# Kernel tuning notes

Hardware: AMD Instinct MI355X
Metric: run time of the kernel (lower is better)

Reference implementation:

```python
import jax, jax.numpy as jnp
import numpy as np

N, M, D = 65536, 1024, 2


def setup_inputs() -> dict:
    key = jax.random.key(0)
    k1, k2, k3 = jax.random.split(key, 3)
    sample = jax.random.uniform(k1, (N, D), dtype=jnp.float32)
    mu = jax.random.uniform(k2, (M, D), dtype=jnp.float32)
    # original init: A = 10 * I; add small noise so covariances are anisotropic
    A = 10.0 * jnp.broadcast_to(jnp.eye(D, dtype=jnp.float32), (M, D, D)) \
        + 0.1 * jax.random.normal(k3, (M, D, D), dtype=jnp.float32)
    w = jnp.ones((M, 1), dtype=jnp.float32)
    return {"sample": sample, "mu": mu, "A": A, "w": w}


def reference(sample, mu, A, w):
    # gamma_j = A_j @ A_j^T  -> precision matrices, (M, D, D)
    gamma = jnp.einsum('mde,mfe->mdf', A, A)
    # 2x2 determinant (only case implemented in the original module)
    det = gamma[:, 0, 0] * gamma[:, 1, 1] - gamma[:, 0, 1] * gamma[:, 1, 0]
    # log weights: log_softmax(w) + 0.5 * log det(gamma)
    log_w = jax.nn.log_softmax(w[:, 0], axis=0) + 0.5 * jnp.log(det)  # (M,)
    # Mahalanobis quadratic form q_ij = (x_i - mu_j)^T gamma_j (x_i - mu_j),
    # expanded to avoid materializing an (N, M, D) difference tensor.
    xGx = jnp.einsum('nd,mde,ne->nm', sample, gamma, sample)          # (N, M)
    gm = jnp.einsum('mde,me->md', gamma, mu)                          # (M, D)
    cross = sample @ gm.T                                             # (N, M)
    mGm = jnp.einsum('md,md->m', gm, mu)                              # (M,)
    q = xGx - 2.0 * cross + mGm[None, :]
    # log-likelihood per sample: logsumexp_j (log_w_j - q_ij)
    return jax.nn.logsumexp(log_w[None, :] - q, axis=1)               # (N,)
```

## Files before the change

### kernel.cpp

```cpp
#include <hip/hip_runtime.h>
#include <math.h>

#define LOG2E 1.4426950408889634f
#define LN2   0.6931471805599453f

static constexpr int M = 1024;
static constexpr int N = 65536;

typedef float v2f __attribute__((ext_vector_type(2)));

__device__ inline v2f pkfma(v2f a, v2f b, v2f c) {
    v2f d;
    asm("v_pk_fma_f32 %0, %1, %2, %3" : "=v"(d) : "v"(a), "v"(b), "v"(c));
    return d;
}

__device__ inline float wave_max64(float v) {
    #pragma unroll
    for (int o = 32; o > 0; o >>= 1) v = fmaxf(v, __shfl_xor(v, o));
    return v;
}
__device__ inline float wave_sum64(float v) {
    #pragma unroll
    for (int o = 32; o > 0; o >>= 1) v += __shfl_xor(v, o);
    return v;
}

__global__ __launch_bounds__(1024)
void gm_all(const float* __restrict__ sample,
            const float* __restrict__ mu,
            const float* __restrict__ A,
            const float* __restrict__ w,
            float* __restrict__ out) {
    __shared__ __align__(16) float coef[M*6];
    __shared__ float partial[16*256];

    const int t    = threadIdx.x;
    const int lane = t & 63;
    const int wv   = t >> 6;
    const int base = blockIdx.x * 256;

    float2 s[4];
    #pragma unroll
    for (int k = 0; k < 4; ++k)
        s[k] = ((const float2*)sample)[base + 64*k + lane];

    const float4 a4  = ((const float4*)A)[t];
    const float2 mu2 = ((const float2*)mu)[t];
    const float  wt  = w[t];

    const float g00 = a4.x*a4.x + a4.y*a4.y;
    const float g01 = a4.x*a4.z + a4.y*a4.w;
    const float g11 = a4.z*a4.z + a4.w*a4.w;
    const float gm0 = g00*mu2.x + g01*mu2.y;
    const float gm1 = g01*mu2.x + g11*mu2.y;
    const float mGm = gm0*mu2.x + gm1*mu2.y;
    const float det = g00*g11 - g01*g01;
    const float t2  = wt*LOG2E + 0.5f*__builtin_amdgcn_logf(det);

    {
        float* c = coef + (t >> 1)*12 + (t & 1);
        c[0]  = t2 - LOG2E * mGm;
        c[2]  = LOG2E * 2.0f * gm0;
        c[4]  = LOG2E * 2.0f * gm1;
        c[6]  = -LOG2E * g00;
        c[8]  = -LOG2E * 2.0f * g01;
        c[10] = -LOG2E * g11;
    }

    float nlse = 0.0f;
    if (wv < 4) {
        float4 wq[4];
        #pragma unroll
        for (int i = 0; i < 4; ++i)
            wq[i] = ((const float4*)w)[lane + 64*i];
        float wmax = wq[0].x;
        #pragma unroll
        for (int i = 0; i < 4; ++i) {
            wmax = fmaxf(wmax, wq[i].x); wmax = fmaxf(wmax, wq[i].y);
            wmax = fmaxf(wmax, wq[i].z); wmax = fmaxf(wmax, wq[i].w);
        }
        wmax = wave_max64(wmax);
        float sw = 0.0f;
        #pragma unroll
        for (int i = 0; i < 4; ++i) {
            sw += __builtin_amdgcn_exp2f((wq[i].x - wmax)*LOG2E);
            sw += __builtin_amdgcn_exp2f((wq[i].y - wmax)*LOG2E);
            sw += __builtin_amdgcn_exp2f((wq[i].z - wmax)*LOG2E);
            sw += __builtin_amdgcn_exp2f((wq[i].w - wmax)*LOG2E);
        }
        sw = wave_sum64(sw);
        nlse = -(wmax*LOG2E + __builtin_amdgcn_logf(sw));
    }

    asm volatile("s_waitcnt lgkmcnt(0)" ::: "memory");
    __builtin_amdgcn_sched_barrier(0);

    v2f X[4], Y[4];
    #pragma unroll
    for (int k = 0; k < 4; ++k) {
        X[k] = (v2f){s[k].x, s[k].x};
        Y[k] = (v2f){s[k].y, s[k].y};
    }
    v2f acc[4] = {(v2f){0,0},(v2f){0,0},(v2f){0,0},(v2f){0,0}};

    const float4* cw = (const float4*)(coef + wv*64*6);
    #pragma unroll 4
    for (int p = 0; p < 32; ++p) {
        const float4 q0 = cw[p*3 + 0];
        const float4 q1 = cw[p*3 + 1];
        const float4 q2 = cw[p*3 + 2];
        const v2f c0 = {q0.x, q0.y}, c1 = {q0.z, q0.w};
        const v2f c2 = {q1.x, q1.y}, c3 = {q1.z, q1.w};
        const v2f c4 = {q2.x, q2.y}, c5 = {q2.z, q2.w};
        #pragma unroll
        for (int k = 0; k < 4; ++k) {
            v2f u  = pkfma(c3, X[k], c1);
            u      = pkfma(c4, Y[k], u);
            v2f t3 = pkfma(c5, Y[k], c2);
            v2f v  = pkfma(u,  X[k], c0);
            v      = pkfma(t3, Y[k], v);
            const float ea = __builtin_amdgcn_exp2f(v.x);
            const float eb = __builtin_amdgcn_exp2f(v.y);
            acc[k] += (v2f){ea, eb};
        }
    }

    #pragma unroll
    for (int k = 0; k < 4; ++k)
        partial[wv*256 + 64*k + lane] = acc[k].x + acc[k].y;
    __syncthreads();

    if (t < 256) {
        float ssum = partial[t];
        #pragma unroll
        for (int i = 1; i < 16; ++i) ssum += partial[i*256 + t];
        out[base + t] = LN2 * (nlse + __builtin_amdgcn_logf(ssum));
    }
}

extern "C" void kernel_launch(void* const* d_in, const int* in_sizes, int n_in,
                              void* d_out, int out_size, void* d_ws, size_t ws_size,
                              hipStream_t stream) {
    const float* sample = (const float*)d_in[0];
    const float* mu     = (const float*)d_in[1];
    const float* A      = (const float*)d_in[2];
    const float* w      = (const float*)d_in[3];
    float* out = (float*)d_out;
    (void)in_sizes; (void)n_in; (void)out_size; (void)d_ws; (void)ws_size;

    gm_all<<<256, 1024, 0, stream>>>(sample, mu, A, w, out);
}
```

Baseline: 70.22 us.

## Compute quadratic forms with bf16 MFMA using hi/lo split features

The per-pair quadratic form is rewritten as a dot product between six polynomial features of each sample (centered at 0.5) and six per-component coefficients. That dot product is evaluated with 16x16x32 bf16 MFMA instructions, using a hi/lo bf16 split of both operands to keep accuracy. This replaces the packed-FMA VALU loop, leaving exp2 and the reductions as the main vector work. It adds LDS staging, a block barrier and cross-lane shuffles, and accuracy depends on the bf16 split and the recentering.

```diff
diff --git a/kernel.cpp b/kernel.cpp
--- a/kernel.cpp
+++ b/kernel.cpp
@@ -7,13 +7,8 @@
 static constexpr int M = 1024;
 static constexpr int N = 65536;
 
-typedef float v2f __attribute__((ext_vector_type(2)));
-
-__device__ inline v2f pkfma(v2f a, v2f b, v2f c) {
-    v2f d;
-    asm("v_pk_fma_f32 %0, %1, %2, %3" : "=v"(d) : "v"(a), "v"(b), "v"(c));
-    return d;
-}
+typedef short bf16x8 __attribute__((ext_vector_type(8)));
+typedef float f32x4  __attribute__((ext_vector_type(4)));
 
 __device__ inline float wave_max64(float v) {
     #pragma unroll
@@ -26,13 +21,21 @@
     return v;
 }
 
+__device__ inline unsigned pk2(float a, float b) {
+    return (__float_as_uint(a) >> 16) | (__float_as_uint(b) & 0xFFFF0000u);
+}
+__device__ inline float truncbf(float f) {
+    return __uint_as_float(__float_as_uint(f) & 0xFFFF0000u);
+}
+
 __global__ __launch_bounds__(1024)
 void gm_all(const float* __restrict__ sample,
             const float* __restrict__ mu,
             const float* __restrict__ A,
             const float* __restrict__ w,
             float* __restrict__ out) {
-    __shared__ __align__(16) float coef[M*6];
+    __shared__ __align__(16) unsigned coefL[M*20];
+    __shared__ __align__(16) unsigned featL[256*20];
     __shared__ float partial[16*256];
 
     const int t    = threadIdx.x;
@@ -40,32 +43,58 @@
     const int wv   = t >> 6;
     const int base = blockIdx.x * 256;
 
-    float2 s[4];
-    #pragma unroll
-    for (int k = 0; k < 4; ++k)
-        s[k] = ((const float2*)sample)[base + 64*k + lane];
-
-    const float4 a4  = ((const float4*)A)[t];
-    const float2 mu2 = ((const float2*)mu)[t];
-    const float  wt  = w[t];
-
-    const float g00 = a4.x*a4.x + a4.y*a4.y;
-    const float g01 = a4.x*a4.z + a4.y*a4.w;
-    const float g11 = a4.z*a4.z + a4.w*a4.w;
-    const float gm0 = g00*mu2.x + g01*mu2.y;
-    const float gm1 = g01*mu2.x + g11*mu2.y;
-    const float mGm = gm0*mu2.x + gm1*mu2.y;
-    const float det = g00*g11 - g01*g01;
-    const float t2  = wt*LOG2E + 0.5f*__builtin_amdgcn_logf(det);
+    {
+        const int s  = t >> 2;
+        const int sl = t & 3;
+        const float2 p = ((const float2*)sample)[base + s];
+        const float x = p.x - 0.5f, y = p.y - 0.5f;
+        const float f0 = 1.0f, f1 = x, f2 = y, f3 = x*x, f4 = x*y, f5 = y*y;
+        const float g0 = f0 - truncbf(f0);
+        const float g1 = f1 - truncbf(f1);
+        const float g2 = f2 - truncbf(f2);
+        const float g3 = f3 - truncbf(f3);
+        const float g4 = f4 - truncbf(f4);
+        const float g5 = f5 - truncbf(f5);
+        const bool lo = (sl & 1);
+        const float v0 = lo ? g0 : f0, v1 = lo ? g1 : f1, v2 = lo ? g2 : f2;
+        const float v3 = lo ? g3 : f3, v4 = lo ? g4 : f4, v5 = lo ? g5 : f5;
+        uint4 q;
+        q.x = pk2(v0, v1); q.y = pk2(v2, v3); q.z = pk2(v4, v5); q.w = 0u;
+        *(uint4*)&featL[s*20 + sl*4] = q;
+    }
 
     {
-        float* c = coef + (t >> 1)*12 + (t & 1);
-        c[0]  = t2 - LOG2E * mGm;
-        c[2]  = LOG2E * 2.0f * gm0;
-        c[4]  = LOG2E * 2.0f * gm1;
-        c[6]  = -LOG2E * g00;
-        c[8]  = -LOG2E * 2.0f * g01;
-        c[10] = -LOG2E * g11;
+        const float4 a4 = ((const float4*)A)[t];
+        const float2 m2 = ((const float2*)mu)[t];
+        const float  wt = w[t];
+        const float g00 = a4.x*a4.x + a4.y*a4.y;
+        const float g01 = a4.x*a4.z + a4.y*a4.w;
+        const float g11 = a4.z*a4.z + a4.w*a4.w;
+        const float gm0 = g00*m2.x + g01*m2.y;
+        const float gm1 = g01*m2.x + g11*m2.y;
+        const float mGm = gm0*m2.x + gm1*m2.y;
+        const float det = g00*g11 - g01*g01;
+        const float t2  = wt*LOG2E + 0.5f*__builtin_amdgcn_logf(det);
+        const float c0o = t2 - LOG2E*mGm;
+        const float c1o = LOG2E*2.0f*gm0;
+        const float c2o = LOG2E*2.0f*gm1;
+        const float c3  = -LOG2E*g00;
+        const float c4  = -LOG2E*2.0f*g01;
+        const float c5  = -LOG2E*g11;
+        const float c1 = c1o + c3 + 0.5f*c4;
+        const float c2 = c2o + c5 + 0.5f*c4;
+        const float c0 = c0o + 0.5f*(c1o + c2o) + 0.25f*(c3 + c4 + c5);
+        const unsigned h0 = pk2(c0, c1), h1 = pk2(c2, c3), h2 = pk2(c4, c5);
+        const float l0 = c0 - truncbf(c0), l1 = c1 - truncbf(c1);
+        const float l2 = c2 - truncbf(c2), l3 = c3 - truncbf(c3);
+        const float l4 = c4 - truncbf(c4), l5 = c5 - truncbf(c5);
+        const unsigned o0 = pk2(l0, l1), o1 = pk2(l2, l3), o2 = pk2(l4, l5);
+        const uint4 hi4 = {h0, h1, h2, 0u};
+        const uint4 lo4 = {o0, o1, o2, 0u};
+        *(uint4*)&coefL[t*20 + 0]  = hi4;
+        *(uint4*)&coefL[t*20 + 4]  = hi4;
+        *(uint4*)&coefL[t*20 + 8]  = lo4;
+        *(uint4*)&coefL[t*20 + 12] = lo4;
     }
 
     float nlse = 0.0f;
@@ -93,42 +122,36 @@
         nlse = -(wmax*LOG2E + __builtin_amdgcn_logf(sw));
     }
 
-    asm volatile("s_waitcnt lgkmcnt(0)" ::: "memory");
-    __builtin_amdgcn_sched_barrier(0);
+    __syncthreads();
 
-    v2f X[4], Y[4];
+    const int l15 = lane & 15;
+    const int ksl = lane >> 4;
+    bf16x8 aA[4];
     #pragma unroll
-    for (int k = 0; k < 4; ++k) {
-        X[k] = (v2f){s[k].x, s[k].x};
-        Y[k] = (v2f){s[k].y, s[k].y};
-    }
-    v2f acc[4] = {(v2f){0,0},(v2f){0,0},(v2f){0,0},(v2f){0,0}};
+    for (int ct = 0; ct < 4; ++ct)
+        aA[ct] = *(const bf16x8*)&coefL[(wv*64 + ct*16 + l15)*20 + ksl*4];
 
-    const float4* cw = (const float4*)(coef + wv*64*6);
-    #pragma unroll 4
-    for (int p = 0; p < 32; ++p) {
-        const float4 q0 = cw[p*3 + 0];
-        const float4 q1 = cw[p*3 + 1];
-        const float4 q2 = cw[p*3 + 2];
-        const v2f c0 = {q0.x, q0.y}, c1 = {q0.z, q0.w};
-        const v2f c2 = {q1.x, q1.y}, c3 = {q1.z, q1.w};
-        const v2f c4 = {q2.x, q2.y}, c5 = {q2.z, q2.w};
-        #pragma unroll
-        for (int k = 0; k < 4; ++k) {
-            v2f u  = pkfma(c3, X[k], c1);
-            u      = pkfma(c4, Y[k], u);
-            v2f t3 = pkfma(c5, Y[k], c2);
-            v2f v  = pkfma(u,  X[k], c0);
-            v      = pkfma(t3, Y[k], v);
-            const float ea = __builtin_amdgcn_exp2f(v.x);
-            const float eb = __builtin_amdgcn_exp2f(v.y);
-            acc[k] += (v2f){ea, eb};
-        }
+    const f32x4 zero4 = {0.0f, 0.0f, 0.0f, 0.0f};
+    for (int st = 0; st < 16; ++st) {
+        const bf16x8 bB = *(const bf16x8*)&featL[(st*16 + l15)*20 + ksl*4];
+        f32x4 d0 = __builtin_amdgcn_mfma_f32_16x16x32_bf16(aA[0], bB, zero4, 0, 0, 0);
+        f32x4 d1 = __builtin_amdgcn_mfma_f32_16x16x32_bf16(aA[1], bB, zero4, 0, 0, 0);
+        f32x4 d2 = __builtin_amdgcn_mfma_f32_16x16x32_bf16(aA[2], bB, zero4, 0, 0, 0);
+        f32x4 d3 = __builtin_amdgcn_mfma_f32_16x16x32_bf16(aA[3], bB, zero4, 0, 0, 0);
+        float s0 = (__builtin_amdgcn_exp2f(d0[0]) + __builtin_amdgcn_exp2f(d0[1]))
+                 + (__builtin_amdgcn_exp2f(d0[2]) + __builtin_amdgcn_exp2f(d0[3]));
+        float s1 = (__builtin_amdgcn_exp2f(d1[0]) + __builtin_amdgcn_exp2f(d1[1]))
+                 + (__builtin_amdgcn_exp2f(d1[2]) + __builtin_amdgcn_exp2f(d1[3]));
+        float s2 = (__builtin_amdgcn_exp2f(d2[0]) + __builtin_amdgcn_exp2f(d2[1]))
+                 + (__builtin_amdgcn_exp2f(d2[2]) + __builtin_amdgcn_exp2f(d2[3]));
+        float s3 = (__builtin_amdgcn_exp2f(d3[0]) + __builtin_amdgcn_exp2f(d3[1]))
+                 + (__builtin_amdgcn_exp2f(d3[2]) + __builtin_amdgcn_exp2f(d3[3]));
+        float s = (s0 + s1) + (s2 + s3);
+        s += __shfl_xor(s, 16);
+        s += __shfl_xor(s, 32);
+        if (ksl == 0) partial[wv*256 + st*16 + l15] = s;
     }
 
-    #pragma unroll
-    for (int k = 0; k < 4; ++k)
-        partial[wv*256 + 64*k + lane] = acc[k].x + acc[k].y;
     __syncthreads();
 
     if (t < 256) {
```

New measurement: 68.06 us. 1.03x faster.
